# Kernel optimization log

Measured on AMD Instinct MI355X. Metric: run time of the kernel, lower is better.

## Reference

```python
import jax, jax.numpy as jnp
import numpy as np

SIGMA = 2.0
INF = 1.0e6
M, N, H, K, C_IN, C_OUT = 50000, 100000, 32, 15, 64, 64
RADIUS = 2.5


def setup_inputs() -> dict:
    key = jax.random.key(0)
    k1, k2, k3, k4, k5, k6 = jax.random.split(key, 6)
    q_points = jax.random.normal(k1, (M, 3), dtype=jnp.float32)
    s_points = jax.random.normal(k2, (N, 3), dtype=jnp.float32)
    s_feats = jax.random.normal(k3, (N, C_IN), dtype=jnp.float32)
    # index N refers to the padding point (placed at INF)
    neighbor_indices = jax.random.randint(k4, (M, H), 0, N + 1, dtype=jnp.int64)
    weights = jax.random.normal(k5, (K, C_IN, C_OUT), dtype=jnp.float32) * 0.05
    # kernel points inside sphere of RADIUS (stand-in for load_kernels buffer)
    kp = jax.random.normal(k6, (K, 3), dtype=jnp.float32)
    kp = kp / jnp.linalg.norm(kp, axis=1, keepdims=True) * RADIUS * 0.7
    kernel_points = kp.at[0].set(0.0)  # fixed='center'
    return {
        "q_points": q_points,
        "s_points": s_points,
        "s_feats": s_feats,
        "neighbor_indices": neighbor_indices,
        "weights": weights,
        "kernel_points": kernel_points,
    }


def reference(q_points, s_points, s_feats, neighbor_indices, weights, kernel_points):
    # pad support points with an 'infinity' shadow point at index N
    padded_pts = jnp.concatenate([s_points, jnp.full((1, 3), INF, s_points.dtype)], axis=0)
    neighbors = padded_pts[neighbor_indices]                    # (M, H, 3)
    rel = neighbors - q_points[:, None, :]                      # (M, H, 3)
    diff = rel[:, :, None, :] - kernel_points[None, None]       # (M, H, K, 3)
    sq_dist = jnp.sum(diff * diff, axis=-1)                     # (M, H, K)
    nbr_w = jnp.clip(1.0 - jnp.sqrt(sq_dist) / SIGMA, 0.0)      # (M, H, K)

    padded_feats = jnp.concatenate([s_feats, jnp.zeros((1, s_feats.shape[1]), s_feats.dtype)], axis=0)
    nbr_feats = padded_feats[neighbor_indices]                  # (M, H, C_in)

    weighted = jnp.einsum('mhk,mhc->mkc', nbr_w, nbr_feats)     # (M, K, C_in)
    out = jnp.einsum('mkc,kcd->md', weighted, weights)          # (M, C_out)

    # normalize by count of real (non-padding / nonzero-sum) neighbors
    nbr_sum = jnp.sum(nbr_feats, axis=-1)                       # (M, H)
    nbr_num = jnp.sum(nbr_sum > 0.0, axis=-1)                   # (M,)
    nbr_num = jnp.maximum(nbr_num, 1)
    return out / nbr_num[:, None].astype(out.dtype)
```

## Files before the change

### kernel.cpp

```cpp
#include <hip/hip_runtime.h>
#include <hip/hip_bf16.h>

#define MPTS 50000
#define NPTS 100000
#define KK 15
#define TM 16
#define WTP 1028
#define STP 36
#define STPH 20

typedef __attribute__((ext_vector_type(8))) short short8;
typedef __attribute__((ext_vector_type(4))) short short4v;
typedef __attribute__((ext_vector_type(4))) float floatx4;

static __device__ __forceinline__ unsigned short f2bf(float f) {
    __hip_bfloat16 h = __float2bfloat16(f);
    return *reinterpret_cast<unsigned short*>(&h);
}

static __device__ __forceinline__ short8 lds_load8(const unsigned short* p) {
    const short4v a = *(const short4v*)p;
    const short4v b = *(const short4v*)(p + 4);
    short8 r;
    r[0] = a[0]; r[1] = a[1]; r[2] = a[2]; r[3] = a[3];
    r[4] = b[0]; r[5] = b[1]; r[6] = b[2]; r[7] = b[3];
    return r;
}

__global__ void prep_all(const float* __restrict__ sf, const float* __restrict__ w,
                         const float* __restrict__ kpts,
                         unsigned short* __restrict__ sfb, float* __restrict__ rs,
                         unsigned short* __restrict__ wbf2, float4* __restrict__ kpp) {
    const int b = blockIdx.x, t = threadIdx.x;
    if (b < 782) {
        const int tt = b * 256 + t;
        const int row = tt >> 1, p = tt & 1;
        if (row < NPTS) {
            const float* base = sf + (size_t)row * 64 + p * 4;
            float4 r = *(const float4*)base;
            {
                ushort4 o;
                o.x = f2bf(r.x); o.y = f2bf(r.y); o.z = f2bf(r.z); o.w = f2bf(r.w);
                *(ushort4*)&sfb[(size_t)row * 64 + p * 4] = o;
            }
#pragma unroll
            for (int i = 1; i < 8; i++) {
                const float4 x = *(const float4*)(base + i * 8);
                ushort4 o;
                o.x = f2bf(x.x); o.y = f2bf(x.y); o.z = f2bf(x.z); o.w = f2bf(x.w);
                *(ushort4*)&sfb[(size_t)row * 64 + i * 8 + p * 4] = o;
                r.x += x.x; r.y += x.y; r.z += x.z; r.w += x.w;
            }
            float sp = (r.x + r.y) + (r.z + r.w);
            sp += __shfl_xor(sp, 1);
            if (p == 0) rs[row] = sp;
        }
    } else if (b < 814) {
        const int e = (b - 782) * 256 + t;
        const int lane = e & 63, s = (e >> 6) & 31, wq = e >> 11;
        const int d = wq * 16 + (lane & 15);
        const int lqp = lane >> 4;
        unsigned short o8[8];
#pragma unroll
        for (int j = 0; j < 8; j++) {
            const int kc = s * 32 + lqp * 8 + j;
            const int c = kc >> 4, k = kc & 15;
            o8[j] = (k < KK) ? f2bf(w[k * 4096 + c * 64 + d]) : (unsigned short)0;
        }
#pragma unroll
        for (int j = 0; j < 8; j++) wbf2[(size_t)e * 8 + j] = o8[j];
    } else {
        if (t < 16) *(ushort4*)&sfb[(size_t)NPTS * 64 + t * 4] = make_ushort4(0, 0, 0, 0);
        else if (t == 16) rs[NPTS] = -1.0f;
        else if (t >= 32 && t < 32 + KK) {
            const int k = t - 32;
            const float kx = kpts[k * 3 + 0], ky = kpts[k * 3 + 1], kz = kpts[k * 3 + 2];
            kpp[k] = make_float4(-2.f * kx, -2.f * ky, -2.f * kz, kx * kx + ky * ky + kz * kz);
        }
    }
}

__global__ __launch_bounds__(512, 6) void kpconv_fused(
    const float* __restrict__ q_points,
    const float* __restrict__ s_points,
    const unsigned short* __restrict__ sfb,
    const int*   __restrict__ nbr,
    const unsigned short* __restrict__ wbf2,
    const float4* __restrict__ kpp,
    const float* __restrict__ rowsum,
    float* __restrict__ out)
{
    const int t    = threadIdx.x;
    const int m0   = blockIdx.x * TM;
    const int lane = t & 63;
    const int wv   = t >> 6;
    const int l15  = lane & 15;
    const int lq   = lane >> 4;

    __shared__ __align__(16) unsigned short stage[8][64 * STPH];
    __shared__ unsigned short wtw[TM * WTP];
    __shared__ float inv_lds[TM];

    const int mw = 2 * wv + (lane >> 5);
    const int h  = lane & 31;

    const int idxp = nbr[(size_t)(m0 + mw) * 32 + h];

    float px = 1.0e6f, py = 1.0e6f, pz = 1.0e6f;
    if (idxp < NPTS) {
        px = s_points[idxp * 3 + 0];
        py = s_points[idxp * 3 + 1];
        pz = s_points[idxp * 3 + 2];
    }

    ushort4 g[2][8];
    const int c4 = l15 * 4;
#pragma unroll
    for (int mi = 0; mi < 2; mi++) {
        const int m = 2 * wv + mi;
#pragma unroll
        for (int g2 = 0; g2 < 4; g2++) {
            const int r0 = g2 * 8 + lq * 2;
            const int2 ip = *(const int2*)&nbr[(size_t)(m0 + m) * 32 + r0];
            const int i0 = min(ip.x, NPTS);
            const int i1 = min(ip.y, NPTS);
            g[mi][2 * g2]     = *(const ushort4*)&sfb[(size_t)i0 * 64 + c4];
            g[mi][2 * g2 + 1] = *(const ushort4*)&sfb[(size_t)i1 * 64 + c4];
        }
    }

    {
        const float rx = px - q_points[(m0 + mw) * 3 + 0];
        const float ry = py - q_points[(m0 + mw) * 3 + 1];
        const float rz = pz - q_points[(m0 + mw) * 3 + 2];
        const float r2 = rx * rx + ry * ry + rz * rz;
        unsigned short* wrow = &wtw[mw * WTP];
#pragma unroll
        for (int k = 0; k < KK; k++) {
            const float4 kp = kpp[k];
            float d2 = kp.w;
            d2 = fmaf(rx, kp.x, d2);
            d2 = fmaf(ry, kp.y, d2);
            d2 = fmaf(rz, kp.z, d2);
            d2 = fmaxf(r2 + d2, 0.0f);
            const float wv_ = fmaxf(fmaf(-0.5f, __builtin_amdgcn_sqrtf(d2), 1.0f), 0.0f);
            wrow[k * STP + h] = f2bf(wv_);
        }
        wrow[15 * STP + h] = 0;

        const bool ok = rowsum[min(idxp, NPTS)] > 0.0f;
        const unsigned long long bal = __ballot(ok);
        if (h == 0) {
            const int cnt = __popc((unsigned)(bal >> ((lane >> 5) * 32)));
            inv_lds[mw] = 1.0f / (float)(cnt < 1 ? 1 : cnt);
        }
    }

    unsigned short* const st = stage[wv];
    const int swzh = (l15 >> 3) << 2;
    const short8 zero8 = {0, 0, 0, 0, 0, 0, 0, 0};
#pragma unroll
    for (int mi = 0; mi < 2; mi++) {
        const int m = 2 * wv + mi;

        const short8 afull = lds_load8(&wtw[m * WTP + l15 * STP + lq * 8]);

        floatx4 d[4];
#pragma unroll
        for (int ct = 0; ct < 4; ct++) d[ct] = (floatx4){0.f, 0.f, 0.f, 0.f};

#pragma unroll
        for (int r = 0; r < 2; r++) {
#pragma unroll
            for (int g2h = 0; g2h < 2; g2h++) {
                const int g2 = 2 * r + g2h;
                const int so = (((g2h * 4 + lq) ^ swzh)) * 2;
                const ushort4 a = g[mi][2 * g2];
                const ushort4 b = g[mi][2 * g2 + 1];
                *(unsigned*)&st[(c4 + 0) * STPH + so] = (unsigned)a.x | ((unsigned)b.x << 16);
                *(unsigned*)&st[(c4 + 1) * STPH + so] = (unsigned)a.y | ((unsigned)b.y << 16);
                *(unsigned*)&st[(c4 + 2) * STPH + so] = (unsigned)a.z | ((unsigned)b.z << 16);
                *(unsigned*)&st[(c4 + 3) * STPH + so] = (unsigned)a.w | ((unsigned)b.w << 16);
            }
            const short8 ar = ((lq >> 1) == r) ? afull : zero8;
#pragma unroll
            for (int ct = 0; ct < 4; ct++) {
                const short8 bfrag =
                    lds_load8(&st[(ct * 16 + l15) * STPH + (((lq & 1) ^ (ct >> 1)) * 8)]);
                d[ct] = __builtin_amdgcn_mfma_f32_16x16x32_bf16(ar, bfrag, d[ct], 0, 0, 0);
            }
        }

#pragma unroll
        for (int ct = 0; ct < 4; ct++) {
            ushort4 pk;
            pk.x = f2bf(d[ct][0]); pk.y = f2bf(d[ct][1]);
            pk.z = f2bf(d[ct][2]); pk.w = f2bf(d[ct][3]);
            *(ushort4*)&wtw[m * WTP + (ct * 16 + l15) * 16 + lq * 4] = pk;
        }
    }
    __syncthreads();

    {
        const int q  = wv & 3;
        const int kh = wv >> 1 >> 1;
        floatx4 acc = {0.f, 0.f, 0.f, 0.f};
        const unsigned short* ap = &wtw[l15 * WTP + kh * 512 + lq * 8];
        const unsigned short* bp = wbf2 + ((size_t)((q * 32 + kh * 16) * 64) + lane) * 8;
#pragma unroll 8
        for (int s = 0; s < 16; s++) {
            const short8 a = lds_load8(ap + s * 32);
            const short8 b = *(const short8*)(bp + s * 512);
            acc = __builtin_amdgcn_mfma_f32_16x16x32_bf16(a, b, acc, 0, 0, 0);
        }

        float* const scratch = (float*)&stage[0][0];
        if (kh == 1) {
            *(floatx4*)&scratch[q * 256 + l15 * 16 + lq * 4] = acc;
        }
        __syncthreads();
        if (kh == 0) {
            const floatx4 p = *(const floatx4*)&scratch[q * 256 + l15 * 16 + lq * 4];
            const int d = q * 16 + l15;
#pragma unroll
            for (int r = 0; r < 4; r++) {
                const int m = lq * 4 + r;
                out[(size_t)(m0 + m) * 64 + d] = (acc[r] + p[r]) * inv_lds[m];
            }
        }
    }
}

extern "C" void kernel_launch(void* const* d_in, const int* in_sizes, int n_in,
                              void* d_out, int out_size, void* d_ws, size_t ws_size,
                              hipStream_t stream) {
    const float* q_points = (const float*)d_in[0];
    const float* s_points = (const float*)d_in[1];
    const float* s_feats  = (const float*)d_in[2];
    const int*   nbr      = (const int*)d_in[3];
    const float* weights  = (const float*)d_in[4];
    const float* kpts     = (const float*)d_in[5];
    float* out = (float*)d_out;

    char* ws = (char*)d_ws;
    unsigned short* wbf2 = (unsigned short*)ws;
    float* rowsum = (float*)(ws + 131072);
    float4* kpp = (float4*)(ws + 531600);
    unsigned short* sfb = (unsigned short*)(ws + 532480);

    prep_all<<<815, 256, 0, stream>>>(s_feats, weights, kpts, sfb, rowsum, wbf2, kpp);
    kpconv_fused<<<MPTS / TM, 512, 0, stream>>>(q_points, s_points, sfb, nbr,
                                                wbf2, kpp, rowsum, out);
}
```

Measured before the change: 142.4 us.

## Make fused kernel persistent over 4 tiles with gather prefetch; pack points with validity flag

Each block now handles four consecutive 16-point tiles. The feature gather for the next tile is issued before the previous tile's output GEMM runs, so global gather latency can overlap with MFMA work. Support-point coordinates and the positive-rowsum flag are packed into one float4 per point during prep, replacing three scalar loads plus a separate rowsum load with a single 16-byte gather. The cost is a grid four times smaller, which lowers the number of resident waves available to hide latency, plus extra barriers inside the tile loop.

```diff
diff --git a/kernel.cpp b/kernel.cpp
--- a/kernel.cpp
+++ b/kernel.cpp
@@ -5,6 +5,9 @@
 #define NPTS 100000
 #define KK 15
 #define TM 16
+#define NTILES (MPTS / TM)
+#define TPB 4
+#define GRID ((NTILES + TPB - 1) / TPB)
 #define WTP 1028
 #define STP 36
 #define STPH 20
@@ -28,8 +31,8 @@
 }
 
 __global__ void prep_all(const float* __restrict__ sf, const float* __restrict__ w,
-                         const float* __restrict__ kpts,
-                         unsigned short* __restrict__ sfb, float* __restrict__ rs,
+                         const float* __restrict__ kpts, const float* __restrict__ spt,
+                         unsigned short* __restrict__ sfb, float4* __restrict__ spts4,
                          unsigned short* __restrict__ wbf2, float4* __restrict__ kpp) {
     const int b = blockIdx.x, t = threadIdx.x;
     if (b < 782) {
@@ -53,7 +56,10 @@
             }
             float sp = (r.x + r.y) + (r.z + r.w);
             sp += __shfl_xor(sp, 1);
-            if (p == 0) rs[row] = sp;
+            if (p == 0) {
+                spts4[row] = make_float4(spt[row * 3 + 0], spt[row * 3 + 1],
+                                         spt[row * 3 + 2], sp > 0.0f ? 1.0f : -1.0f);
+            }
         }
     } else if (b < 814) {
         const int e = (b - 782) * 256 + t;
@@ -71,7 +77,7 @@
         for (int j = 0; j < 8; j++) wbf2[(size_t)e * 8 + j] = o8[j];
     } else {
         if (t < 16) *(ushort4*)&sfb[(size_t)NPTS * 64 + t * 4] = make_ushort4(0, 0, 0, 0);
-        else if (t == 16) rs[NPTS] = -1.0f;
+        else if (t == 16) spts4[NPTS] = make_float4(1.0e6f, 1.0e6f, 1.0e6f, -1.0f);
         else if (t >= 32 && t < 32 + KK) {
             const int k = t - 32;
             const float kx = kpts[k * 3 + 0], ky = kpts[k * 3 + 1], kz = kpts[k * 3 + 2];
@@ -82,16 +88,14 @@
 
 __global__ __launch_bounds__(512, 6) void kpconv_fused(
     const float* __restrict__ q_points,
-    const float* __restrict__ s_points,
+    const float4* __restrict__ spts4,
     const unsigned short* __restrict__ sfb,
     const int*   __restrict__ nbr,
     const unsigned short* __restrict__ wbf2,
     const float4* __restrict__ kpp,
-    const float* __restrict__ rowsum,
     float* __restrict__ out)
 {
     const int t    = threadIdx.x;
-    const int m0   = blockIdx.x * TM;
     const int lane = t & 63;
     const int wv   = t >> 6;
     const int l15  = lane & 15;
@@ -103,36 +107,39 @@
 
     const int mw = 2 * wv + (lane >> 5);
     const int h  = lane & 31;
-
-    const int idxp = nbr[(size_t)(m0 + mw) * 32 + h];
-
-    float px = 1.0e6f, py = 1.0e6f, pz = 1.0e6f;
-    if (idxp < NPTS) {
-        px = s_points[idxp * 3 + 0];
-        py = s_points[idxp * 3 + 1];
-        pz = s_points[idxp * 3 + 2];
-    }
+    const int c4 = l15 * 4;
 
     ushort4 g[2][8];
-    const int c4 = l15 * 4;
-#pragma unroll
-    for (int mi = 0; mi < 2; mi++) {
-        const int m = 2 * wv + mi;
-#pragma unroll
-        for (int g2 = 0; g2 < 4; g2++) {
-            const int r0 = g2 * 8 + lq * 2;
-            const int2 ip = *(const int2*)&nbr[(size_t)(m0 + m) * 32 + r0];
-            const int i0 = min(ip.x, NPTS);
-            const int i1 = min(ip.y, NPTS);
-            g[mi][2 * g2]     = *(const ushort4*)&sfb[(size_t)i0 * 64 + c4];
-            g[mi][2 * g2 + 1] = *(const ushort4*)&sfb[(size_t)i1 * 64 + c4];
-        }
-    }
-
-    {
-        const float rx = px - q_points[(m0 + mw) * 3 + 0];
-        const float ry = py - q_points[(m0 + mw) * 3 + 1];
-        const float rz = pz - q_points[(m0 + mw) * 3 + 2];
+    float4 sp4;
+
+    const int q  = wv & 3;
+    const int kh = wv >> 2;
+    const unsigned short* const ap = &wtw[l15 * WTP + kh * 512 + lq * 8];
+    const unsigned short* const bp = wbf2 + ((size_t)((q * 32 + kh * 16) * 64) + lane) * 8;
+    float* const scratch = (float*)&stage[0][0];
+
+    auto PREFETCH = [&](const int m0n) {
+        const int idxp = nbr[(size_t)(m0n + mw) * 32 + h];
+#pragma unroll
+        for (int mi = 0; mi < 2; mi++) {
+            const int m = 2 * wv + mi;
+#pragma unroll
+            for (int g2 = 0; g2 < 4; g2++) {
+                const int r0 = g2 * 8 + lq * 2;
+                const int2 ip = *(const int2*)&nbr[(size_t)(m0n + m) * 32 + r0];
+                const int i0 = min(ip.x, NPTS);
+                const int i1 = min(ip.y, NPTS);
+                g[mi][2 * g2]     = *(const ushort4*)&sfb[(size_t)i0 * 64 + c4];
+                g[mi][2 * g2 + 1] = *(const ushort4*)&sfb[(size_t)i1 * 64 + c4];
+            }
+        }
+        sp4 = spts4[min(idxp, NPTS)];
+    };
+
+    auto WEIGHTS = [&](const int m0c) {
+        const float rx = sp4.x - q_points[(m0c + mw) * 3 + 0];
+        const float ry = sp4.y - q_points[(m0c + mw) * 3 + 1];
+        const float rz = sp4.z - q_points[(m0c + mw) * 3 + 2];
         const float r2 = rx * rx + ry * ry + rz * rz;
         unsigned short* wrow = &wtw[mw * WTP];
 #pragma unroll
@@ -148,73 +155,63 @@
         }
         wrow[15 * STP + h] = 0;
 
-        const bool ok = rowsum[min(idxp, NPTS)] > 0.0f;
-        const unsigned long long bal = __ballot(ok);
+        const unsigned long long bal = __ballot(sp4.w > 0.0f);
         if (h == 0) {
             const int cnt = __popc((unsigned)(bal >> ((lane >> 5) * 32)));
             inv_lds[mw] = 1.0f / (float)(cnt < 1 ? 1 : cnt);
         }
-    }
+    };
 
     unsigned short* const st = stage[wv];
     const int swzh = (l15 >> 3) << 2;
     const short8 zero8 = {0, 0, 0, 0, 0, 0, 0, 0};
-#pragma unroll
-    for (int mi = 0; mi < 2; mi++) {
-        const int m = 2 * wv + mi;
-
-        const short8 afull = lds_load8(&wtw[m * WTP + l15 * STP + lq * 8]);
-
-        floatx4 d[4];
-#pragma unroll
-        for (int ct = 0; ct < 4; ct++) d[ct] = (floatx4){0.f, 0.f, 0.f, 0.f};
-
-#pragma unroll
-        for (int r = 0; r < 2; r++) {
-#pragma unroll
-            for (int g2h = 0; g2h < 2; g2h++) {
-                const int g2 = 2 * r + g2h;
-                const int so = (((g2h * 4 + lq) ^ swzh)) * 2;
-                const ushort4 a = g[mi][2 * g2];
-                const ushort4 b = g[mi][2 * g2 + 1];
-                *(unsigned*)&st[(c4 + 0) * STPH + so] = (unsigned)a.x | ((unsigned)b.x << 16);
-                *(unsigned*)&st[(c4 + 1) * STPH + so] = (unsigned)a.y | ((unsigned)b.y << 16);
-                *(unsigned*)&st[(c4 + 2) * STPH + so] = (unsigned)a.z | ((unsigned)b.z << 16);
-                *(unsigned*)&st[(c4 + 3) * STPH + so] = (unsigned)a.w | ((unsigned)b.w << 16);
-            }
-            const short8 ar = ((lq >> 1) == r) ? afull : zero8;
+    auto PHASEB = [&]() {
+#pragma unroll
+        for (int mi = 0; mi < 2; mi++) {
+            const int m = 2 * wv + mi;
+            const short8 afull = lds_load8(&wtw[m * WTP + l15 * STP + lq * 8]);
+            floatx4 d[4];
+#pragma unroll
+            for (int ct = 0; ct < 4; ct++) d[ct] = (floatx4){0.f, 0.f, 0.f, 0.f};
+#pragma unroll
+            for (int r = 0; r < 2; r++) {
+#pragma unroll
+                for (int g2h = 0; g2h < 2; g2h++) {
+                    const int g2 = 2 * r + g2h;
+                    const int so = (((g2h * 4 + lq) ^ swzh)) * 2;
+                    const ushort4 a = g[mi][2 * g2];
+                    const ushort4 b = g[mi][2 * g2 + 1];
+                    *(unsigned*)&st[(c4 + 0) * STPH + so] = (unsigned)a.x | ((unsigned)b.x << 16);
+                    *(unsigned*)&st[(c4 + 1) * STPH + so] = (unsigned)a.y | ((unsigned)b.y << 16);
+                    *(unsigned*)&st[(c4 + 2) * STPH + so] = (unsigned)a.z | ((unsigned)b.z << 16);
+                    *(unsigned*)&st[(c4 + 3) * STPH + so] = (unsigned)a.w | ((unsigned)b.w << 16);
+                }
+                const short8 ar = ((lq >> 1) == r) ? afull : zero8;
+#pragma unroll
+                for (int ct = 0; ct < 4; ct++) {
+                    const short8 bfrag =
+                        lds_load8(&st[(ct * 16 + l15) * STPH + (((lq & 1) ^ (ct >> 1)) * 8)]);
+                    d[ct] = __builtin_amdgcn_mfma_f32_16x16x32_bf16(ar, bfrag, d[ct], 0, 0, 0);
+                }
+            }
 #pragma unroll
             for (int ct = 0; ct < 4; ct++) {
-                const short8 bfrag =
-                    lds_load8(&st[(ct * 16 + l15) * STPH + (((lq & 1) ^ (ct >> 1)) * 8)]);
-                d[ct] = __builtin_amdgcn_mfma_f32_16x16x32_bf16(ar, bfrag, d[ct], 0, 0, 0);
-            }
-        }
-
-#pragma unroll
-        for (int ct = 0; ct < 4; ct++) {
-            ushort4 pk;
-            pk.x = f2bf(d[ct][0]); pk.y = f2bf(d[ct][1]);
-            pk.z = f2bf(d[ct][2]); pk.w = f2bf(d[ct][3]);
-            *(ushort4*)&wtw[m * WTP + (ct * 16 + l15) * 16 + lq * 4] = pk;
-        }
-    }
-    __syncthreads();
-
-    {
-        const int q  = wv & 3;
-        const int kh = wv >> 1 >> 1;
+                ushort4 pk;
+                pk.x = f2bf(d[ct][0]); pk.y = f2bf(d[ct][1]);
+                pk.z = f2bf(d[ct][2]); pk.w = f2bf(d[ct][3]);
+                *(ushort4*)&wtw[m * WTP + (ct * 16 + l15) * 16 + lq * 4] = pk;
+            }
+        }
+    };
+
+    auto PHASEC = [&](const int m0p) {
         floatx4 acc = {0.f, 0.f, 0.f, 0.f};
-        const unsigned short* ap = &wtw[l15 * WTP + kh * 512 + lq * 8];
-        const unsigned short* bp = wbf2 + ((size_t)((q * 32 + kh * 16) * 64) + lane) * 8;
 #pragma unroll 8
         for (int s = 0; s < 16; s++) {
             const short8 a = lds_load8(ap + s * 32);
             const short8 b = *(const short8*)(bp + s * 512);
             acc = __builtin_amdgcn_mfma_f32_16x16x32_bf16(a, b, acc, 0, 0, 0);
         }
-
-        float* const scratch = (float*)&stage[0][0];
         if (kh == 1) {
             *(floatx4*)&scratch[q * 256 + l15 * 16 + lq * 4] = acc;
         }
@@ -225,10 +222,26 @@
 #pragma unroll
             for (int r = 0; r < 4; r++) {
                 const int m = lq * 4 + r;
-                out[(size_t)(m0 + m) * 64 + d] = (acc[r] + p[r]) * inv_lds[m];
-            }
-        }
+                out[(size_t)(m0p + m) * 64 + d] = (acc[r] + p[r]) * inv_lds[m];
+            }
+        }
+    };
+
+    const int tile0 = blockIdx.x * TPB;
+    const int nt = min(TPB, NTILES - tile0);
+    PREFETCH(tile0 * TM);
+    int m0p = 0;
+    for (int i = 0; i < nt; i++) {
+        const int m0c = (tile0 + i) * TM;
+        if (i > 0) PHASEC(m0p);
+        __syncthreads();
+        WEIGHTS(m0c);
+        PHASEB();
+        if (i + 1 < nt) PREFETCH(m0c + TM);
+        __syncthreads();
+        m0p = m0c;
     }
+    PHASEC(m0p);
 }
 
 extern "C" void kernel_launch(void* const* d_in, const int* in_sizes, int n_in,
@@ -244,11 +257,12 @@
 
     char* ws = (char*)d_ws;
     unsigned short* wbf2 = (unsigned short*)ws;
-    float* rowsum = (float*)(ws + 131072);
-    float4* kpp = (float4*)(ws + 531600);
-    unsigned short* sfb = (unsigned short*)(ws + 532480);
-
-    prep_all<<<815, 256, 0, stream>>>(s_feats, weights, kpts, sfb, rowsum, wbf2, kpp);
-    kpconv_fused<<<MPTS / TM, 512, 0, stream>>>(q_points, s_points, sfb, nbr,
-                                                wbf2, kpp, rowsum, out);
-}
+    float4* spts4 = (float4*)(ws + 131072);
+    float4* kpp = (float4*)(ws + 1731088);
+    unsigned short* sfb = (unsigned short*)(ws + 1731584);
+
+    prep_all<<<815, 256, 0, stream>>>(s_feats, weights, kpts, s_points,
+                                      sfb, spts4, wbf2, kpp);
+    kpconv_fused<<<GRID, 512, 0, stream>>>(q_points, spts4, sfb, nbr,
+                                           wbf2, kpp, out);
+}
```

New measurement: 179.3 us. +25.9%, slower.

## Quantize support features to int8 with per-row scale folded into kernel weights

Applied to the files above, without the earlier changes.

The prep kernel now quantizes each support-feature row to signed int8 with a per-row absmax scale, instead of converting it to bf16. It also packs point coordinates, the scale and the positive-row-sum sign into one float4 per point. The main kernel gathers 4-byte uchar4 instead of 8-byte ushort4 feature chunks and makes one float4 load per neighbor instead of separate coordinate and rowsum loads. It folds the row scale into the bf16 kernel-point weight before the MFMA, which halves gather bandwidth at the cost of int8 quantization error and extra convert instructions. Launch bounds drop from 6 to 2 waves per EU.

```diff
diff --git a/kernel.cpp b/kernel.cpp
--- a/kernel.cpp
+++ b/kernel.cpp
@@ -27,9 +27,13 @@
     return r;
 }
 
+static __device__ __forceinline__ unsigned cvtb(unsigned char u) {
+    return (unsigned)f2bf((float)(int)(signed char)u);
+}
+
 __global__ void prep_all(const float* __restrict__ sf, const float* __restrict__ w,
-                         const float* __restrict__ kpts,
-                         unsigned short* __restrict__ sfb, float* __restrict__ rs,
+                         const float* __restrict__ kpts, const float* __restrict__ spt,
+                         unsigned char* __restrict__ sfb8, float4* __restrict__ spts4,
                          unsigned short* __restrict__ wbf2, float4* __restrict__ kpp) {
     const int b = blockIdx.x, t = threadIdx.x;
     if (b < 782) {
@@ -37,23 +41,36 @@
         const int row = tt >> 1, p = tt & 1;
         if (row < NPTS) {
             const float* base = sf + (size_t)row * 64 + p * 4;
-            float4 r = *(const float4*)base;
-            {
-                ushort4 o;
-                o.x = f2bf(r.x); o.y = f2bf(r.y); o.z = f2bf(r.z); o.w = f2bf(r.w);
-                *(ushort4*)&sfb[(size_t)row * 64 + p * 4] = o;
-            }
+            float4 x[8];
+            x[0] = *(const float4*)base;
+            float4 r = x[0];
+            float am = fmaxf(fmaxf(fabsf(x[0].x), fabsf(x[0].y)),
+                             fmaxf(fabsf(x[0].z), fabsf(x[0].w)));
 #pragma unroll
             for (int i = 1; i < 8; i++) {
-                const float4 x = *(const float4*)(base + i * 8);
-                ushort4 o;
-                o.x = f2bf(x.x); o.y = f2bf(x.y); o.z = f2bf(x.z); o.w = f2bf(x.w);
-                *(ushort4*)&sfb[(size_t)row * 64 + i * 8 + p * 4] = o;
-                r.x += x.x; r.y += x.y; r.z += x.z; r.w += x.w;
+                x[i] = *(const float4*)(base + i * 8);
+                r.x += x[i].x; r.y += x[i].y; r.z += x[i].z; r.w += x[i].w;
+                am = fmaxf(am, fmaxf(fmaxf(fabsf(x[i].x), fabsf(x[i].y)),
+                                     fmaxf(fabsf(x[i].z), fabsf(x[i].w))));
             }
             float sp = (r.x + r.y) + (r.z + r.w);
             sp += __shfl_xor(sp, 1);
-            if (p == 0) rs[row] = sp;
+            am = fmaxf(am, __shfl_xor(am, 1));
+            const float inv = am > 0.0f ? 127.0f / am : 0.0f;
+#pragma unroll
+            for (int i = 0; i < 8; i++) {
+                uchar4 o;
+                o.x = (unsigned char)(int)rintf(x[i].x * inv);
+                o.y = (unsigned char)(int)rintf(x[i].y * inv);
+                o.z = (unsigned char)(int)rintf(x[i].z * inv);
+                o.w = (unsigned char)(int)rintf(x[i].w * inv);
+                *(uchar4*)&sfb8[(size_t)row * 64 + i * 8 + p * 4] = o;
+            }
+            if (p == 0) {
+                const float sc = am * (1.0f / 127.0f);
+                spts4[row] = make_float4(spt[row * 3 + 0], spt[row * 3 + 1],
+                                         spt[row * 3 + 2], sp > 0.0f ? sc : -sc);
+            }
         }
     } else if (b < 814) {
         const int e = (b - 782) * 256 + t;
@@ -70,8 +87,8 @@
 #pragma unroll
         for (int j = 0; j < 8; j++) wbf2[(size_t)e * 8 + j] = o8[j];
     } else {
-        if (t < 16) *(ushort4*)&sfb[(size_t)NPTS * 64 + t * 4] = make_ushort4(0, 0, 0, 0);
-        else if (t == 16) rs[NPTS] = -1.0f;
+        if (t < 16) *(uchar4*)&sfb8[(size_t)NPTS * 64 + t * 4] = make_uchar4(0, 0, 0, 0);
+        else if (t == 16) spts4[NPTS] = make_float4(1.0e6f, 1.0e6f, 1.0e6f, -1.0f);
         else if (t >= 32 && t < 32 + KK) {
             const int k = t - 32;
             const float kx = kpts[k * 3 + 0], ky = kpts[k * 3 + 1], kz = kpts[k * 3 + 2];
@@ -80,14 +97,13 @@
     }
 }
 
-__global__ __launch_bounds__(512, 6) void kpconv_fused(
+__global__ __launch_bounds__(512, 2) void kpconv_fused(
     const float* __restrict__ q_points,
-    const float* __restrict__ s_points,
-    const unsigned short* __restrict__ sfb,
+    const float4* __restrict__ spts4,
+    const unsigned char* __restrict__ sfb8,
     const int*   __restrict__ nbr,
     const unsigned short* __restrict__ wbf2,
     const float4* __restrict__ kpp,
-    const float* __restrict__ rowsum,
     float* __restrict__ out)
 {
     const int t    = threadIdx.x;
@@ -103,18 +119,12 @@
 
     const int mw = 2 * wv + (lane >> 5);
     const int h  = lane & 31;
+    const int c4 = l15 * 4;
 
     const int idxp = nbr[(size_t)(m0 + mw) * 32 + h];
-
-    float px = 1.0e6f, py = 1.0e6f, pz = 1.0e6f;
-    if (idxp < NPTS) {
-        px = s_points[idxp * 3 + 0];
-        py = s_points[idxp * 3 + 1];
-        pz = s_points[idxp * 3 + 2];
-    }
-
-    ushort4 g[2][8];
-    const int c4 = l15 * 4;
+    const float4 sp4 = spts4[min(idxp, NPTS)];
+
+    uchar4 g[2][8];
 #pragma unroll
     for (int mi = 0; mi < 2; mi++) {
         const int m = 2 * wv + mi;
@@ -124,16 +134,17 @@
             const int2 ip = *(const int2*)&nbr[(size_t)(m0 + m) * 32 + r0];
             const int i0 = min(ip.x, NPTS);
             const int i1 = min(ip.y, NPTS);
-            g[mi][2 * g2]     = *(const ushort4*)&sfb[(size_t)i0 * 64 + c4];
-            g[mi][2 * g2 + 1] = *(const ushort4*)&sfb[(size_t)i1 * 64 + c4];
+            g[mi][2 * g2]     = *(const uchar4*)&sfb8[(size_t)i0 * 64 + c4];
+            g[mi][2 * g2 + 1] = *(const uchar4*)&sfb8[(size_t)i1 * 64 + c4];
         }
     }
 
     {
-        const float rx = px - q_points[(m0 + mw) * 3 + 0];
-        const float ry = py - q_points[(m0 + mw) * 3 + 1];
-        const float rz = pz - q_points[(m0 + mw) * 3 + 2];
+        const float rx = sp4.x - q_points[(m0 + mw) * 3 + 0];
+        const float ry = sp4.y - q_points[(m0 + mw) * 3 + 1];
+        const float rz = sp4.z - q_points[(m0 + mw) * 3 + 2];
         const float r2 = rx * rx + ry * ry + rz * rz;
+        const float ss = fabsf(sp4.w);
         unsigned short* wrow = &wtw[mw * WTP];
 #pragma unroll
         for (int k = 0; k < KK; k++) {
@@ -144,12 +155,11 @@
             d2 = fmaf(rz, kp.z, d2);
             d2 = fmaxf(r2 + d2, 0.0f);
             const float wv_ = fmaxf(fmaf(-0.5f, __builtin_amdgcn_sqrtf(d2), 1.0f), 0.0f);
-            wrow[k * STP + h] = f2bf(wv_);
+            wrow[k * STP + h] = f2bf(wv_ * ss);
         }
         wrow[15 * STP + h] = 0;
 
-        const bool ok = rowsum[min(idxp, NPTS)] > 0.0f;
-        const unsigned long long bal = __ballot(ok);
+        const unsigned long long bal = __ballot(sp4.w > 0.0f);
         if (h == 0) {
             const int cnt = __popc((unsigned)(bal >> ((lane >> 5) * 32)));
             inv_lds[mw] = 1.0f / (float)(cnt < 1 ? 1 : cnt);
@@ -162,25 +172,22 @@
 #pragma unroll
     for (int mi = 0; mi < 2; mi++) {
         const int m = 2 * wv + mi;
-
         const short8 afull = lds_load8(&wtw[m * WTP + l15 * STP + lq * 8]);
-
         floatx4 d[4];
 #pragma unroll
         for (int ct = 0; ct < 4; ct++) d[ct] = (floatx4){0.f, 0.f, 0.f, 0.f};
-
 #pragma unroll
         for (int r = 0; r < 2; r++) {
 #pragma unroll
             for (int g2h = 0; g2h < 2; g2h++) {
                 const int g2 = 2 * r + g2h;
                 const int so = (((g2h * 4 + lq) ^ swzh)) * 2;
-                const ushort4 a = g[mi][2 * g2];
-                const ushort4 b = g[mi][2 * g2 + 1];
-                *(unsigned*)&st[(c4 + 0) * STPH + so] = (unsigned)a.x | ((unsigned)b.x << 16);
-                *(unsigned*)&st[(c4 + 1) * STPH + so] = (unsigned)a.y | ((unsigned)b.y << 16);
-                *(unsigned*)&st[(c4 + 2) * STPH + so] = (unsigned)a.z | ((unsigned)b.z << 16);
-                *(unsigned*)&st[(c4 + 3) * STPH + so] = (unsigned)a.w | ((unsigned)b.w << 16);
+                const uchar4 a = g[mi][2 * g2];
+                const uchar4 b = g[mi][2 * g2 + 1];
+                *(unsigned*)&st[(c4 + 0) * STPH + so] = cvtb(a.x) | (cvtb(b.x) << 16);
+                *(unsigned*)&st[(c4 + 1) * STPH + so] = cvtb(a.y) | (cvtb(b.y) << 16);
+                *(unsigned*)&st[(c4 + 2) * STPH + so] = cvtb(a.z) | (cvtb(b.z) << 16);
+                *(unsigned*)&st[(c4 + 3) * STPH + so] = cvtb(a.w) | (cvtb(b.w) << 16);
             }
             const short8 ar = ((lq >> 1) == r) ? afull : zero8;
 #pragma unroll
@@ -190,7 +197,6 @@
                 d[ct] = __builtin_amdgcn_mfma_f32_16x16x32_bf16(ar, bfrag, d[ct], 0, 0, 0);
             }
         }
-
 #pragma unroll
         for (int ct = 0; ct < 4; ct++) {
             ushort4 pk;
@@ -203,7 +209,7 @@
 
     {
         const int q  = wv & 3;
-        const int kh = wv >> 1 >> 1;
+        const int kh = wv >> 2;
         floatx4 acc = {0.f, 0.f, 0.f, 0.f};
         const unsigned short* ap = &wtw[l15 * WTP + kh * 512 + lq * 8];
         const unsigned short* bp = wbf2 + ((size_t)((q * 32 + kh * 16) * 64) + lane) * 8;
@@ -244,11 +250,12 @@
 
     char* ws = (char*)d_ws;
     unsigned short* wbf2 = (unsigned short*)ws;
-    float* rowsum = (float*)(ws + 131072);
-    float4* kpp = (float4*)(ws + 531600);
-    unsigned short* sfb = (unsigned short*)(ws + 532480);
-
-    prep_all<<<815, 256, 0, stream>>>(s_feats, weights, kpts, sfb, rowsum, wbf2, kpp);
-    kpconv_fused<<<MPTS / TM, 512, 0, stream>>>(q_points, s_points, sfb, nbr,
-                                                wbf2, kpp, rowsum, out);
-}
+    float4* spts4 = (float4*)(ws + 131072);
+    float4* kpp = (float4*)(ws + 1731088);
+    unsigned char* sfb8 = (unsigned char*)(ws + 1731584);
+
+    prep_all<<<815, 256, 0, stream>>>(s_feats, weights, kpts, s_points,
+                                      sfb8, spts4, wbf2, kpp);
+    kpconv_fused<<<MPTS / TM, 512, 0, stream>>>(q_points, spts4, sfb8, nbr,
+                                                wbf2, kpp, out);
+}
```

New measurement: 133.4 us (median of 2 runs). 1.07x faster.
